# Optimization experiments

Measured on AMD Instinct MI355X. Metric: run time of the kernel, lower is better.

The kernel has to match this reference:

```python
import jax, jax.numpy as jnp
import numpy as np

B, T, C, H = 8, 2048, 768, 64  # batch, seq, n_embed, head_size

def setup_inputs() -> dict:
    key = jax.random.key(0)
    kx, kq, kk, kv = jax.random.split(key, 4)
    x = jax.random.normal(kx, (B, T, C), dtype=jnp.float32)
    Wq = jax.random.normal(kq, (C, H), dtype=jnp.float32) * (C ** -0.5)
    Wk = jax.random.normal(kk, (C, H), dtype=jnp.float32) * (C ** -0.5)
    Wv = jax.random.normal(kv, (C, H), dtype=jnp.float32) * (C ** -0.5)
    return {"x": x, "Wq": Wq, "Wk": Wk, "Wv": Wv}

def reference(x, Wq, Wk, Wv):
    # projections (bias-free linears)
    q = jnp.einsum('btc,ch->bth', x, Wq)
    k = jnp.einsum('btc,ch->bth', x, Wk)
    v = jnp.einsum('btc,ch->bth', x, Wv)
    scale = k.shape[-1] ** -0.5
    wei = jnp.einsum('bth,bsh->bts', q, k) * scale  # [B, T, T]
    Tq = x.shape[1]
    causal = jnp.tril(jnp.ones((Tq, Tq), dtype=bool))
    wei = jnp.where(causal, wei, -jnp.inf)
    wei = jax.nn.softmax(wei, axis=-1)
    # dropout p=0.0 -> identity
    out = jnp.einsum('bts,bsh->bth', wei, v)
    return out
```

## Files before the change

### kernel.cpp

```cpp
#include <hip/hip_runtime.h>


typedef __bf16 bf16x8 __attribute__((ext_vector_type(8)));
typedef float  f32x4  __attribute__((ext_vector_type(4)));
typedef unsigned int u32;

union ABu {
    bf16x8 v;
    uint4  u;
    unsigned short us[8];
};

__device__ __forceinline__ unsigned short f2bf(float f) {
    union { __bf16 h; unsigned short s; } c;
    c.h = (__bf16)f;
    return c.s;
}
__device__ __forceinline__ float bf2f(unsigned short s) {
    union { unsigned int u; float f; } c; c.u = ((unsigned int)s) << 16;
    return c.f;
}
__device__ __forceinline__ u32 cvtpk_bf16(float lo, float hi) {
    u32 r;
    asm("v_cvt_pk_bf16_f32 %0, %1, %2" : "=v"(r) : "v"(lo), "v"(hi));
    return r;
}

__device__ __forceinline__ void gld16(void* lds, const void* g) {
    __builtin_amdgcn_global_load_lds(
        (const u32 __attribute__((address_space(1)))*)g,
        (u32 __attribute__((address_space(3)))*)lds, 16, 0, 0);
}

__global__ __launch_bounds__(256)
void wt_kernel(const float* __restrict__ Wq, const float* __restrict__ Wk,
               const float* __restrict__ Wv, unsigned short* __restrict__ wF) {
    const int j   = blockIdx.x / 6;
    const int kgg = blockIdx.x % 6;
    const int t = threadIdx.x;
    const int kg = kgg * 4 + (t >> 6);
    const int lane = t & 63, quad = lane >> 4, l16 = lane & 15;
    const int m = j >> 2, nb = (j & 3) * 16;
    const float* W = (m == 0) ? Wq : (m == 1) ? Wk : Wv;
    ABu o;
#pragma unroll
    for (int i = 0; i < 8; ++i)
        o.us[i] = f2bf(W[(kg * 32 + quad * 8 + i) * 64 + nb + l16]);
    *(uint4*)(wF + ((size_t)(j * 24 + kg) * 64 + lane) * 8) = o.u;
}

__global__ __launch_bounds__(512, 4)
void qkv_kernel(const float* __restrict__ x, const unsigned short* __restrict__ wF,
                unsigned short* __restrict__ qF, unsigned short* __restrict__ kF,
                unsigned short* __restrict__ vF) {
    __shared__ unsigned short xs[2][32][72];
    __shared__ unsigned short wsW[2][24][64][8];
    __shared__ unsigned short Cst[2][12][16][17];
    const int tid  = threadIdx.x;
    const int lane = tid & 63, w = tid >> 6;
    const int l16  = lane & 15, quad = lane >> 4;
    const int mh   = w & 1, nh = w >> 1;
    const int m0   = blockIdx.x * 32;
    const int b    = m0 >> 11;

    f32x4 acc[3];
#pragma unroll
    for (int j = 0; j < 3; ++j) acc[j] = (f32x4){0.f, 0.f, 0.f, 0.f};

    const int xrow = tid >> 4, xc16 = tid & 15;

#pragma unroll
    for (int i = 0; i < 3; ++i) {
        const int c = w * 3 + i, j = c >> 1, kg2 = c & 1;
        gld16((char*)wsW[0] + (size_t)c * 1024 + lane * 16,
              (const char*)wF + ((size_t)(j * 24 + kg2) * 64 + lane) * 16);
    }
    {
        float4 xv = *(const float4*)&x[(size_t)(m0 + xrow) * 768 + xc16 * 4];
        *(uint2*)&xs[0][xrow][xc16 * 4] =
            (uint2){cvtpk_bf16(xv.x, xv.y), cvtpk_bf16(xv.z, xv.w)};
    }
    __syncthreads();

    for (int kk = 0; kk < 12; ++kk) {
        const int cur = kk & 1, nxt = cur ^ 1;
        float4 xn;
        if (kk + 1 < 12) {
#pragma unroll
            for (int i = 0; i < 3; ++i) {
                const int c = w * 3 + i, j = c >> 1, kg2 = c & 1;
                gld16((char*)wsW[nxt] + (size_t)c * 1024 + lane * 16,
                      (const char*)wF + ((size_t)(j * 24 + (kk + 1) * 2 + kg2) * 64 + lane) * 16);
            }
            xn = *(const float4*)&x[(size_t)(m0 + xrow) * 768 + (kk + 1) * 64 + xc16 * 4];
        }

#pragma unroll
        for (int kg2 = 0; kg2 < 2; ++kg2) {
            ABu af;
            af.u = *(const uint4*)&xs[cur][mh * 16 + l16][kg2 * 32 + quad * 8];
#pragma unroll
            for (int jl = 0; jl < 3; ++jl) {
                const int j = nh * 3 + jl;
                ABu bf;
                bf.u = *(const uint4*)((char*)wsW[cur] + (size_t)(j * 2 + kg2) * 1024 + lane * 16);
                acc[jl] = __builtin_amdgcn_mfma_f32_16x16x32_bf16(af.v, bf.v, acc[jl], 0, 0, 0);
            }
        }

        if (kk + 1 < 12)
            *(uint2*)&xs[nxt][xrow][xc16 * 4] =
                (uint2){cvtpk_bf16(xn.x, xn.y), cvtpk_bf16(xn.z, xn.w)};
        __syncthreads();
    }

#pragma unroll
    for (int jl = 0; jl < 3; ++jl)
#pragma unroll
        for (int r = 0; r < 4; ++r)
            Cst[mh][nh * 3 + jl][quad * 4 + r][l16] = f2bf(acc[jl][r]);
    __syncthreads();

    const int g = tid >> 6, el = tid & 63;
    const int eq = el >> 4, e16 = el & 15;
    if (g < 4) {
        const int mhh = g >> 1, kg = g & 1;
        ABu oq, ok;
#pragma unroll
        for (int i = 0; i < 8; ++i) {
            const int h = kg * 32 + eq * 8 + i;
            oq.us[i] = Cst[mhh][h >> 4][e16][h & 15];
            ok.us[i] = Cst[mhh][4 + (h >> 4)][e16][h & 15];
        }
        const size_t tt = (size_t)b * 128 + ((m0 & 2047) >> 4) + mhh;
        *(uint4*)(qF + ((tt * 2 + kg) * 64 + el) * 8) = oq.u;
        *(uint4*)(kF + ((tt * 2 + kg) * 64 + el) * 8) = ok.u;
    } else {
        const int nt = g & 3;
        const int sv = (m0 & 2047) >> 6, kg = (m0 >> 5) & 1;
        ABu ov;
#pragma unroll
        for (int i = 0; i < 8; ++i) {
            const int loc = eq * 8 + i;
            ov.us[i] = Cst[loc >> 4][8 + nt][loc & 15][e16];
        }
        *(uint4*)(vF + ((((size_t)(b * 32 + sv) * 4 + nt) * 2 + kg) * 64 + el) * 8) = ov.u;
    }
}

template<bool MASKED>
__device__ __forceinline__ void attn_tile(
    const int st, const int b, const int tq0,
    const int lane, const int l16, const int quad,
    const ABu& aq0, const ABu& aq1, const ABu& onesb,
    const unsigned short* __restrict__ kF,
    const unsigned short* __restrict__ vF,
    f32x4 acc[4], f32x4& lacc)
{
    const float SC = 0.125f * 1.44269504089f;
    const float MB = 16.0f  * 1.44269504089f;
    const int s0 = st * 64;
    const unsigned short* kbase = kF + (size_t)(b * 128 + st * 4) * 1024;
    const unsigned short* vbase = vF + (size_t)(b * 32 + st) * 4096;

    ABu kf[8];
#pragma unroll
    for (int c = 0; c < 8; ++c)
        kf[c].u = *(const uint4*)(kbase + (size_t)c * 512 + lane * 8);
    ABu vf[8];
#pragma unroll
    for (int c = 0; c < 8; ++c)
        vf[c].u = *(const uint4*)(vbase + (size_t)c * 512 + lane * 8);

    float p[4][4];
#pragma unroll
    for (int nt = 0; nt < 4; ++nt) {
        f32x4 s = (f32x4){0.f, 0.f, 0.f, 0.f};
        s = __builtin_amdgcn_mfma_f32_16x16x32_bf16(kf[nt * 2 + 0].v, aq0.v, s, 0, 0, 0);
        s = __builtin_amdgcn_mfma_f32_16x16x32_bf16(kf[nt * 2 + 1].v, aq1.v, s, 0, 0, 0);
#pragma unroll
        for (int r = 0; r < 4; ++r) {
            float pv = __builtin_amdgcn_exp2f(__builtin_fmaf(s[r], SC, -MB));
            if (MASKED)
                pv = (s0 + nt * 16 + quad * 4 + r > tq0 + l16) ? 0.f : pv;
            p[nt][r] = pv;
        }
    }

    ABu af[2];
#pragma unroll
    for (int ks = 0; ks < 2; ++ks) {
        u32 x0 = cvtpk_bf16(p[2 * ks][0], p[2 * ks][1]);
        u32 x1 = cvtpk_bf16(p[2 * ks][2], p[2 * ks][3]);
        u32 y0 = cvtpk_bf16(p[2 * ks + 1][0], p[2 * ks + 1][1]);
        u32 y1 = cvtpk_bf16(p[2 * ks + 1][2], p[2 * ks + 1][3]);
        asm("v_permlane32_swap_b32 %0, %1" : "+v"(x0), "+v"(y0));
        asm("v_permlane16_swap_b32 %0, %1" : "+v"(x0), "+v"(y0));
        asm("v_permlane32_swap_b32 %0, %1" : "+v"(x1), "+v"(y1));
        asm("v_permlane16_swap_b32 %0, %1" : "+v"(x1), "+v"(y1));
        af[ks].u = (uint4){x0, x1, y0, y1};
    }

#pragma unroll
    for (int nt = 0; nt < 4; ++nt) {
        acc[nt] = __builtin_amdgcn_mfma_f32_16x16x32_bf16(af[0].v, vf[nt * 2 + 0].v, acc[nt], 0, 0, 0);
        acc[nt] = __builtin_amdgcn_mfma_f32_16x16x32_bf16(af[1].v, vf[nt * 2 + 1].v, acc[nt], 0, 0, 0);
    }
    lacc = __builtin_amdgcn_mfma_f32_16x16x32_bf16(af[0].v, onesb.v, lacc, 0, 0, 0);
    lacc = __builtin_amdgcn_mfma_f32_16x16x32_bf16(af[1].v, onesb.v, lacc, 0, 0, 0);
}

__global__ __launch_bounds__(256, 2)
void attn_kernel(const unsigned short* __restrict__ qF,
                 const unsigned short* __restrict__ kF,
                 const unsigned short* __restrict__ vF,
                 unsigned short* __restrict__ opart, float* __restrict__ lpart) {
    const int tid  = threadIdx.x;
    const int lane = tid & 63, w = tid >> 6;
    const int l16  = lane & 15, quad = lane >> 4;
    const int idx  = blockIdx.x;
    const int b    = idx & 7;
    const int hi   = idx >> 3;
    const int quarter = hi & 3;
    const int g    = (hi >> 2) & 7;
    const int tr   = hi >> 5;
    const int v    = g + ((tr >> 1) << 3);
    const int qs   = (tr & 1) ? (31 - v) : v;
    const int tt   = qs * 4 + w;
    const int tq0  = tt * 16;

    ABu aq0, aq1, onesb;
    aq0.u = *(const uint4*)(qF + ((((size_t)b * 128 + tt) * 2 + 0) * 64 + lane) * 8);
    aq1.u = *(const uint4*)(qF + ((((size_t)b * 128 + tt) * 2 + 1) * 64 + lane) * 8);
    onesb.u = (uint4){0x3F803F80u, 0x3F803F80u, 0x3F803F80u, 0x3F803F80u};

    f32x4 acc[4];
#pragma unroll
    for (int nt = 0; nt < 4; ++nt) acc[nt] = (f32x4){0.f, 0.f, 0.f, 0.f};
    f32x4 lacc = (f32x4){0.f, 0.f, 0.f, 0.f};

    int st = quarter;
    for (; st < qs; st += 4)
        attn_tile<false>(st, b, tq0, lane, l16, quad, aq0, aq1, onesb, kF, vF, acc, lacc);
    if (st == qs)
        attn_tile<true>(st, b, tq0, lane, l16, quad, aq0, aq1, onesb, kF, vF, acc, lacc);

    unsigned short* obase = opart + ((size_t)(quarter * 8 + b) * 2048 + tq0) * 64;
#pragma unroll
    for (int nt = 0; nt < 4; ++nt)
#pragma unroll
        for (int r = 0; r < 4; ++r)
            obase[(size_t)(quad * 4 + r) * 64 + nt * 16 + l16] = f2bf(acc[nt][r]);
    if (l16 == 0) {
#pragma unroll
        for (int r = 0; r < 4; ++r)
            lpart[(size_t)(quarter * 8 + b) * 2048 + tq0 + quad * 4 + r] = lacc[r];
    }
}

__global__ __launch_bounds__(256)
void finalize_kernel(const unsigned short* __restrict__ opart,
                     const float* __restrict__ lpart, float* __restrict__ out) {
    const int idx = blockIdx.x * 256 + threadIdx.x;
    const int row = idx >> 4;
    float4 v = (float4){0.f, 0.f, 0.f, 0.f};
    float  l = 0.f;
#pragma unroll
    for (int q = 0; q < 4; ++q) {
        ushort4 u = ((const ushort4*)opart)[(size_t)q * 262144 + idx];
        v.x += bf2f(u.x); v.y += bf2f(u.y); v.z += bf2f(u.z); v.w += bf2f(u.w);
        l += lpart[(size_t)q * 16384 + row];
    }
    const float li = 1.f / l;
    v.x *= li; v.y *= li; v.z *= li; v.w *= li;
    ((float4*)out)[idx] = v;
}

extern "C" void kernel_launch(void* const* d_in, const int* in_sizes, int n_in,
                              void* d_out, int out_size, void* d_ws, size_t ws_size,
                              hipStream_t stream) {
    const float* x  = (const float*)d_in[0];
    const float* Wq = (const float*)d_in[1];
    const float* Wk = (const float*)d_in[2];
    const float* Wv = (const float*)d_in[3];
    float* out = (float*)d_out;

    char* ws = (char*)d_ws;
    unsigned short* wF    = (unsigned short*)ws;
    unsigned short* qF    = (unsigned short*)(ws + (512 << 10));
    unsigned short* kF    = (unsigned short*)(ws + (512 << 10) + (2 << 20));
    unsigned short* vF    = (unsigned short*)(ws + (512 << 10) + (4 << 20));
    unsigned short* opart = (unsigned short*)(ws + (512 << 10) + (6 << 20));
    float*          lpart = (float*)(ws + (512 << 10) + (14 << 20));

    wt_kernel<<<72, 256, 0, stream>>>(Wq, Wk, Wv, wF);
    qkv_kernel<<<512, 512, 0, stream>>>(x, wF, qF, kF, vF);
    attn_kernel<<<1024, 256, 0, stream>>>(qF, kF, vF, opart, lpart);
    finalize_kernel<<<1024, 256, 0, stream>>>(opart, lpart, out);
}
```

Before: 117.2 us.

## Fuse split-K finalize into attention kernel via last-block atomic counter

Removes the separate finalize kernel launch. Each attention block increments a per-(batch, query-tile) atomic counter, and the fourth block to finish sums the four partial outputs and normalizers and writes the final fp32 output. The counters are zeroed in the weight-transpose kernel. This saves one launch and its pass over the partials, in exchange for fences, atomics and a reduction tail done by only some blocks.

```diff
diff --git a/kernel.cpp b/kernel.cpp
--- a/kernel.cpp
+++ b/kernel.cpp
@@ -34,10 +34,12 @@
 
 __global__ __launch_bounds__(256)
 void wt_kernel(const float* __restrict__ Wq, const float* __restrict__ Wk,
-               const float* __restrict__ Wv, unsigned short* __restrict__ wF) {
+               const float* __restrict__ Wv, unsigned short* __restrict__ wF,
+               int* __restrict__ cnt) {
+    const int t = threadIdx.x;
+    if (blockIdx.x == 0) cnt[t] = 0;
     const int j   = blockIdx.x / 6;
     const int kgg = blockIdx.x % 6;
-    const int t = threadIdx.x;
     const int kg = kgg * 4 + (t >> 6);
     const int lane = t & 63, quad = lane >> 4, l16 = lane & 15;
     const int m = j >> 2, nb = (j & 3) * 16;
@@ -214,7 +216,9 @@
 void attn_kernel(const unsigned short* __restrict__ qF,
                  const unsigned short* __restrict__ kF,
                  const unsigned short* __restrict__ vF,
-                 unsigned short* __restrict__ opart, float* __restrict__ lpart) {
+                 unsigned short* __restrict__ opart, float* __restrict__ lpart,
+                 int* __restrict__ cnt, float* __restrict__ out) {
+    __shared__ int s_old;
     const int tid  = threadIdx.x;
     const int lane = tid & 63, w = tid >> 6;
     const int l16  = lane & 15, quad = lane >> 4;
@@ -256,24 +260,43 @@
         for (int r = 0; r < 4; ++r)
             lpart[(size_t)(quarter * 8 + b) * 2048 + tq0 + quad * 4 + r] = lacc[r];
     }
-}
-
-__global__ __launch_bounds__(256)
-void finalize_kernel(const unsigned short* __restrict__ opart,
-                     const float* __restrict__ lpart, float* __restrict__ out) {
-    const int idx = blockIdx.x * 256 + threadIdx.x;
-    const int row = idx >> 4;
-    float4 v = (float4){0.f, 0.f, 0.f, 0.f};
-    float  l = 0.f;
-#pragma unroll
-    for (int q = 0; q < 4; ++q) {
-        ushort4 u = ((const ushort4*)opart)[(size_t)q * 262144 + idx];
-        v.x += bf2f(u.x); v.y += bf2f(u.y); v.z += bf2f(u.z); v.w += bf2f(u.w);
-        l += lpart[(size_t)q * 16384 + row];
-    }
-    const float li = 1.f / l;
-    v.x *= li; v.y *= li; v.z *= li; v.w *= li;
-    ((float4*)out)[idx] = v;
+
+    __threadfence();
+    __syncthreads();
+    if (tid == 0) s_old = atomicAdd(&cnt[b * 32 + qs], 1);
+    __syncthreads();
+    if (s_old == 3) {
+        __threadfence();
+        const int r  = tid >> 2;
+        const int cg = (tid & 3) * 16;
+        const int t  = qs * 64 + r;
+        float l = 0.f;
+#pragma unroll
+        for (int q = 0; q < 4; ++q) l += lpart[(size_t)(q * 8 + b) * 2048 + t];
+        const float li = 1.f / l;
+        float s[16];
+#pragma unroll
+        for (int i = 0; i < 16; ++i) s[i] = 0.f;
+#pragma unroll
+        for (int q = 0; q < 4; ++q) {
+            const unsigned short* pp = opart + ((size_t)(q * 8 + b) * 2048 + t) * 64 + cg;
+            uint4 u0 = *(const uint4*)pp;
+            uint4 u1 = *(const uint4*)(pp + 8);
+            const unsigned short* us0 = (const unsigned short*)&u0;
+            const unsigned short* us1 = (const unsigned short*)&u1;
+#pragma unroll
+            for (int i = 0; i < 8; ++i) {
+                s[i]     += bf2f(us0[i]);
+                s[8 + i] += bf2f(us1[i]);
+            }
+        }
+        float* op = out + ((size_t)b * 2048 + t) * 64 + cg;
+#pragma unroll
+        for (int i = 0; i < 16; ++i) s[i] *= li;
+#pragma unroll
+        for (int i = 0; i < 4; ++i)
+            *(float4*)(op + i * 4) = (float4){s[i * 4], s[i * 4 + 1], s[i * 4 + 2], s[i * 4 + 3]};
+    }
 }
 
 extern "C" void kernel_launch(void* const* d_in, const int* in_sizes, int n_in,
@@ -292,9 +315,9 @@
     unsigned short* vF    = (unsigned short*)(ws + (512 << 10) + (4 << 20));
     unsigned short* opart = (unsigned short*)(ws + (512 << 10) + (6 << 20));
     float*          lpart = (float*)(ws + (512 << 10) + (14 << 20));
-
-    wt_kernel<<<72, 256, 0, stream>>>(Wq, Wk, Wv, wF);
+    int*            cnt   = (int*)(ws + (512 << 10) + (14 << 20) + (256 << 10));
+
+    wt_kernel<<<72, 256, 0, stream>>>(Wq, Wk, Wv, wF, cnt);
     qkv_kernel<<<512, 512, 0, stream>>>(x, wF, qF, kF, vF);
-    attn_kernel<<<1024, 256, 0, stream>>>(qF, kF, vF, opart, lpart);
-    finalize_kernel<<<1024, 256, 0, stream>>>(opart, lpart, out);
-}
+    attn_kernel<<<1024, 256, 0, stream>>>(qF, kF, vF, opart, lpart, cnt, out);
+}
```

Result: slower. 266.5 us (+127.3%).

## Load QKV projection operands directly from global memory, dropping LDS staging

Applied to the files above, without the earlier changes.

The QKV projection kernel no longer stages x and the packed weights through double-buffered shared memory with global_load_lds and per-step barriers. Each lane now loads its own x fragment and weight fragment straight from global memory into registers, converts x to bf16 in registers, and feeds the MFMA. This removes the LDS traffic and the 12 block-wide syncs. In exchange, x rows are read redundantly by the 4 waves that share an mh, global loads are no longer prefetched one step ahead, and load latency may be exposed.

```diff
diff --git a/kernel.cpp b/kernel.cpp
--- a/kernel.cpp
+++ b/kernel.cpp
@@ -24,12 +24,6 @@
     u32 r;
     asm("v_cvt_pk_bf16_f32 %0, %1, %2" : "=v"(r) : "v"(lo), "v"(hi));
     return r;
-}
-
-__device__ __forceinline__ void gld16(void* lds, const void* g) {
-    __builtin_amdgcn_global_load_lds(
-        (const u32 __attribute__((address_space(1)))*)g,
-        (u32 __attribute__((address_space(3)))*)lds, 16, 0, 0);
 }
 
 __global__ __launch_bounds__(256)
@@ -53,8 +47,6 @@
 void qkv_kernel(const float* __restrict__ x, const unsigned short* __restrict__ wF,
                 unsigned short* __restrict__ qF, unsigned short* __restrict__ kF,
                 unsigned short* __restrict__ vF) {
-    __shared__ unsigned short xs[2][32][72];
-    __shared__ unsigned short wsW[2][24][64][8];
     __shared__ unsigned short Cst[2][12][16][17];
     const int tid  = threadIdx.x;
     const int lane = tid & 63, w = tid >> 6;
@@ -67,51 +59,27 @@
 #pragma unroll
     for (int j = 0; j < 3; ++j) acc[j] = (f32x4){0.f, 0.f, 0.f, 0.f};
 
-    const int xrow = tid >> 4, xc16 = tid & 15;
-
-#pragma unroll
-    for (int i = 0; i < 3; ++i) {
-        const int c = w * 3 + i, j = c >> 1, kg2 = c & 1;
-        gld16((char*)wsW[0] + (size_t)c * 1024 + lane * 16,
-              (const char*)wF + ((size_t)(j * 24 + kg2) * 64 + lane) * 16);
-    }
-    {
-        float4 xv = *(const float4*)&x[(size_t)(m0 + xrow) * 768 + xc16 * 4];
-        *(uint2*)&xs[0][xrow][xc16 * 4] =
-            (uint2){cvtpk_bf16(xv.x, xv.y), cvtpk_bf16(xv.z, xv.w)};
-    }
-    __syncthreads();
+    const float* xr = x + (size_t)(m0 + mh * 16 + l16) * 768 + quad * 8;
+    const unsigned short* wb = wF + lane * 8;
 
     for (int kk = 0; kk < 12; ++kk) {
-        const int cur = kk & 1, nxt = cur ^ 1;
-        float4 xn;
-        if (kk + 1 < 12) {
-#pragma unroll
-            for (int i = 0; i < 3; ++i) {
-                const int c = w * 3 + i, j = c >> 1, kg2 = c & 1;
-                gld16((char*)wsW[nxt] + (size_t)c * 1024 + lane * 16,
-                      (const char*)wF + ((size_t)(j * 24 + (kk + 1) * 2 + kg2) * 64 + lane) * 16);
-            }
-            xn = *(const float4*)&x[(size_t)(m0 + xrow) * 768 + (kk + 1) * 64 + xc16 * 4];
-        }
-
 #pragma unroll
         for (int kg2 = 0; kg2 < 2; ++kg2) {
+            float4 f0 = *(const float4*)(xr + kk * 64 + kg2 * 32);
+            float4 f1 = *(const float4*)(xr + kk * 64 + kg2 * 32 + 4);
             ABu af;
-            af.u = *(const uint4*)&xs[cur][mh * 16 + l16][kg2 * 32 + quad * 8];
+            af.u.x = cvtpk_bf16(f0.x, f0.y);
+            af.u.y = cvtpk_bf16(f0.z, f0.w);
+            af.u.z = cvtpk_bf16(f1.x, f1.y);
+            af.u.w = cvtpk_bf16(f1.z, f1.w);
 #pragma unroll
             for (int jl = 0; jl < 3; ++jl) {
-                const int j = nh * 3 + jl;
                 ABu bf;
-                bf.u = *(const uint4*)((char*)wsW[cur] + (size_t)(j * 2 + kg2) * 1024 + lane * 16);
+                bf.u = *(const uint4*)(wb +
+                    ((size_t)(nh * 3 + jl) * 24 + kk * 2 + kg2) * 512);
                 acc[jl] = __builtin_amdgcn_mfma_f32_16x16x32_bf16(af.v, bf.v, acc[jl], 0, 0, 0);
             }
         }
-
-        if (kk + 1 < 12)
-            *(uint2*)&xs[nxt][xrow][xc16 * 4] =
-                (uint2){cvtpk_bf16(xn.x, xn.y), cvtpk_bf16(xn.z, xn.w)};
-        __syncthreads();
     }
 
 #pragma unroll
```

Measured after the change: 133.3 us. 13.8% more time.
